# Performance work log

Hardware: AMD Instinct MI355X
Metric: run time of the kernel (lower is better)

## Reference

```python
import jax, jax.numpy as jnp
import numpy as np

T = 3              # num_ntype (slots)
NH = 64            # num_hidden == num_classes
HEADS = (4, 4, 1)
NUM_ETYPES = 5
EDGE_DIM = 64
N_NODES = 20000
NEG_SLOPE = 0.2
ALPHA = 0.05       # residual-attention blend
EPS = 1e-12


def _l2_by_slot(x):
    # l2_norm with l2BySlot='True': normalize each ntype slot independently
    n = x.shape[0]
    xs = x.reshape(n, T, -1)
    nrm = jnp.linalg.norm(xs, axis=2, keepdims=True)
    return (xs / jnp.maximum(nrm, EPS)).reshape(n, -1)


def _edge_softmax(logits, dst, n):
    # softmax over incoming edges of each destination node
    m = jax.lax.stop_gradient(jax.ops.segment_max(logits, dst, num_segments=n))
    e = jnp.exp(logits - m[dst])
    s = jax.ops.segment_sum(e, dst, num_segments=n)
    return e / s[dst]


def _conv(x, src, dst, etype, W, al, ar, ee_tab, We, ae, res_attn, act):
    # slotGATConv: x [N,T,C], W [T,C,H*O], al/ar [H,T*O], ee_tab [R,De], We [De,H*De], ae [H,De]
    n = x.shape[0]
    H = al.shape[0]
    proj = jnp.einsum('ntc,tcd->ntd', x, W)                     # [N,T,H*O]
    O = proj.shape[-1] // H
    feat = proj.reshape(n, T, H, O).transpose(0, 2, 1, 3).reshape(n, H, T * O)
    el = jnp.einsum('nhd,hd->nh', feat, al)
    er = jnp.einsum('nhd,hd->nh', feat, ar)
    De = ee_tab.shape[1]
    ep = (ee_tab[etype] @ We).reshape(-1, H, De)                # [E,H,De]
    ee = jnp.einsum('ehd,hd->eh', ep, ae)                       # [E,H]
    logit = jax.nn.leaky_relu(el[src] + er[dst] + ee, NEG_SLOPE)
    a = _edge_softmax(logit, dst, n)                            # [E,H]
    if res_attn is not None:
        a = a * (1.0 - ALPHA) + res_attn * ALPHA
    out = jax.ops.segment_sum(feat[src] * a[:, :, None], dst, num_segments=n)  # [N,H,T*O]
    if act:
        out = jax.nn.elu(out)
    return out, a


def _forward(feat0, feat1, feat2, w_in0, b_in0, w_in1, b_in1, w_in2, b_in2,
             l0_W, l0_al, l0_ar, l0_ee, l0_we, l0_ae,
             l1_W, l1_al, l1_ar, l1_ee, l1_we, l1_ae,
             l2_W, l2_al, l2_ar, l2_ee, l2_we, l2_ae,
             dm_W, e_feat, src, dst, left, right, mid):
    feats = [feat0, feat1, feat2]
    lins = [(w_in0, b_in0), (w_in1, b_in1), (w_in2, b_in2)]
    blocks = []
    for t, (f, (w, b)) in enumerate(zip(feats, lins)):
        ft = f @ w + b                                          # [n_t, NH]
        pad = jnp.zeros((f.shape[0], T * NH), ft.dtype)
        blocks.append(pad.at[:, t * NH:(t + 1) * NH].set(ft))   # slot zero-padding
    h = jnp.concatenate(blocks, 0)                              # [N, T*NH]
    emb = [_l2_by_slot(h)]                                      # aggregator='None' -> identity
    x = h.reshape(-1, T, NH)
    out0, a0 = _conv(x, src, dst, e_feat, l0_W, l0_al, l0_ar, l0_ee, l0_we, l0_ae, None, True)
    emb.append(_l2_by_slot(out0.mean(1)))
    x = out0.reshape(-1, HEADS[0], T, NH).transpose(0, 2, 1, 3).reshape(-1, T, HEADS[0] * NH)
    out1, a1 = _conv(x, src, dst, e_feat, l1_W, l1_al, l1_ar, l1_ee, l1_we, l1_ae, a0, True)
    emb.append(_l2_by_slot(out1.mean(1)))
    x = out1.reshape(-1, HEADS[1], T, NH).transpose(0, 2, 1, 3).reshape(-1, T, HEADS[1] * NH)
    out2, _ = _conv(x, src, dst, e_feat, l2_W, l2_al, l2_ar, l2_ee, l2_we, l2_ae, a1, False)
    emb.append(_l2_by_slot(out2.mean(1)))
    # aggregator='None' + inProcessEmb='True': concat per-slot along feature dim
    embs = [e.reshape(-1, T, NH) for e in emb]
    o = jnp.concatenate(embs, 2).reshape(-1, T * NH * len(embs))  # [N, 768]
    le, re = o[left], o[right]
    scores = jnp.zeros(left.shape[0], o.dtype)
    for r in range(NUM_ETYPES):                                 # DistMult per relation
        s = ((le @ dm_W[r]) * re).sum(1)
        scores = jnp.where(mid == r, s, scores)
    return jax.nn.sigmoid(scores)


def setup_inputs() -> dict:
    key = jax.random.key(0)
    ks = iter(jax.random.split(key, 64))
    def nrm(shape, std):
        return jax.random.normal(next(ks), shape, jnp.float32) * std
    counts = [8000, 6000, 6000]
    in_dims = [256, 128, 64]
    inp = {}
    for t in range(T):
        inp[f'feat{t}'] = jax.random.normal(next(ks), (counts[t], in_dims[t]), jnp.float32)
        inp[f'w_in{t}'] = nrm((in_dims[t], NH), 0.1)
        inp[f'b_in{t}'] = nrm((NH,), 0.1)
    Cs = [NH, HEADS[0] * NH, HEADS[1] * NH]
    for l in range(3):
        H = HEADS[l]
        inp[f'l{l}_W'] = nrm((T, Cs[l], H * NH), 0.1)
        inp[f'l{l}_al'] = nrm((H, T * NH), 0.1)
        inp[f'l{l}_ar'] = nrm((H, T * NH), 0.1)
        inp[f'l{l}_ee'] = nrm((NUM_ETYPES, EDGE_DIM), 0.1)
        inp[f'l{l}_we'] = nrm((EDGE_DIM, H * EDGE_DIM), 0.1)
        inp[f'l{l}_ae'] = nrm((H, EDGE_DIM), 0.1)
    D = T * NH * 4
    inp['dm_W'] = nrm((NUM_ETYPES, D, D), 0.05)
    E, L = 200000, 10000
    inp['e_feat'] = jax.random.randint(next(ks), (E,), 0, NUM_ETYPES)
    inp['src'] = jax.random.randint(next(ks), (E,), 0, N_NODES)
    inp['dst'] = jax.random.randint(next(ks), (E,), 0, N_NODES)
    inp['left'] = jax.random.randint(next(ks), (L,), 0, N_NODES)
    inp['right'] = jax.random.randint(next(ks), (L,), 0, N_NODES)
    inp['mid'] = jax.random.randint(next(ks), (L,), 0, NUM_ETYPES)
    return inp


def reference(feat0, feat1, feat2, w_in0, b_in0, w_in1, b_in1, w_in2, b_in2,
              l0_W, l0_al, l0_ar, l0_ee, l0_we, l0_ae,
              l1_W, l1_al, l1_ar, l1_ee, l1_we, l1_ae,
              l2_W, l2_al, l2_ar, l2_ee, l2_we, l2_ae,
              dm_W, e_feat, src, dst, left, right, mid):
    return _forward(feat0, feat1, feat2, w_in0, b_in0, w_in1, b_in1, w_in2, b_in2,
                    l0_W, l0_al, l0_ar, l0_ee, l0_we, l0_ae,
                    l1_W, l1_al, l1_ar, l1_ee, l1_we, l1_ae,
                    l2_W, l2_al, l2_ar, l2_ee, l2_we, l2_ae,
                    dm_W, e_feat, src, dst, left, right, mid)
```

## Files before the change

kernel.cpp:

```cpp
#include <hip/hip_runtime.h>
#include <math.h>

#define N_NODES 20000
#define NPAD    20096
#define N_EDGES 200000
#define N_PAIRS 10000
#define PAIR_PAD 10368
#define DM_TILES 162
#define NBLK    79

typedef __attribute__((ext_vector_type(8))) short s16x8;
typedef __attribute__((ext_vector_type(4))) float f32x4;

__device__ inline float wave_max(float v){
  for (int o = 32; o > 0; o >>= 1) v = fmaxf(v, __shfl_xor(v, o));
  return v;
}
__device__ inline float wave_sum(float v){
  for (int o = 32; o > 0; o >>= 1) v += __shfl_xor(v, o);
  return v;
}
__device__ inline short f2bf(float x){
  union { float f; unsigned u; } v; v.f = x;
  unsigned r = (v.u + 0x7FFFu + ((v.u >> 16) & 1u)) >> 16;
  return (short)r;
}
__device__ inline float bf2f(short s){
  union { unsigned u; float f; } v; v.u = ((unsigned)(unsigned short)s) << 16;
  return v.f;
}

__global__ void build_h(const float* __restrict__ f0, const float* __restrict__ w0, const float* __restrict__ b0,
                        const float* __restrict__ f1, const float* __restrict__ w1, const float* __restrict__ b1,
                        const float* __restrict__ f2, const float* __restrict__ w2, const float* __restrict__ b2,
                        short* __restrict__ Xb0, short* __restrict__ o_b){
  int n = blockIdx.x, lane = threadIdx.x;
  int t, idx, C; const float *f, *w, *b;
  if (n < 8000)       { t = 0; idx = n;         C = 256; f = f0; w = w0; b = b0; }
  else if (n < 14000) { t = 1; idx = n - 8000;  C = 128; f = f1; w = w1; b = b1; }
  else                { t = 2; idx = n - 14000; C = 64;  f = f2; w = w2; b = b2; }
  __shared__ float xs[256];
  for (int c = lane; c < C; c += 64) xs[c] = f[(size_t)idx * C + c];
  __syncthreads();
  float acc = b[lane];
  for (int c = 0; c < C; c++) acc += xs[c] * w[c * 64 + lane];
  for (int tt = 0; tt < 3; tt++)
    Xb0[((size_t)(tt * NPAD) + n) * 64 + lane] = f2bf((tt == t) ? acc : 0.f);
  float ss = wave_sum(acc * acc);
  float sc = 1.f / fmaxf(sqrtf(ss), 1e-12f);
  for (int tt = 0; tt < 3; tt++)
    o_b[(size_t)n * 768 + tt * 256 + lane] = f2bf((tt == t) ? acc * sc : 0.f);
}

__global__ void zero_init(int* __restrict__ csr_cnt, int* __restrict__ cnt5, int* __restrict__ pos5,
                          float* __restrict__ score, int* __restrict__ pairs,
                          short* __restrict__ Xb0, short* __restrict__ Xb12){
  int i = blockIdx.x * 256 + threadIdx.x;
  if (i < N_NODES) csr_cnt[i] = 0;
  if (i < 5) { cnt5[i * 16] = 0; pos5[i * 16] = 0; }
  if (i < N_PAIRS) score[i] = 0.f;
  if (i < PAIR_PAD) pairs[i] = -1;
  s16x8 z = {};
  if (i < 4608){
    int t = (i * 16) / 24576, off = (i * 16) % 24576;
    short* p = Xb12 + ((size_t)(t * NPAD + N_NODES)) * 256 + off;
    *(s16x8*)p = z; *(s16x8*)(p + 8) = z;
  }
  if (i < 1152){
    int t = (i * 16) / 6144, off = (i * 16) % 6144;
    short* p = Xb0 + ((size_t)(t * NPAD + N_NODES)) * 64 + off;
    *(s16x8*)p = z; *(s16x8*)(p + 8) = z;
  }
}

__global__ void count_k(const int* __restrict__ dst, int* __restrict__ csr_cnt,
                        const int* __restrict__ mid, int* __restrict__ cnt5){
  int e = blockIdx.x * 256 + threadIdx.x;
  int lane = threadIdx.x & 63;
  if (e < N_EDGES) atomicAdd(&csr_cnt[dst[e]], 1);
  int r_mine = (e < N_PAIRS) ? mid[e] : -1;
#pragma unroll
  for (int r = 0; r < 5; r++){
    unsigned long long mask = __ballot(r_mine == r);
    if (mask){
      int leader = __ffsll((long long)mask) - 1;
      if (lane == leader) atomicAdd(&cnt5[r * 16], __popcll(mask));
    }
  }
}

__global__ void scan1_k(const int* __restrict__ cnt, int* __restrict__ loc, int* __restrict__ bsum){
  __shared__ int s[256];
  int tid = threadIdx.x;
  int idx = blockIdx.x * 256 + tid;
  int v = (idx < N_NODES) ? cnt[idx] : 0;
  s[tid] = v;
  __syncthreads();
  for (int o = 1; o < 256; o <<= 1){
    int u = (tid >= o) ? s[tid - o] : 0;
    __syncthreads();
    s[tid] += u;
    __syncthreads();
  }
  if (idx < N_NODES) loc[idx] = s[tid] - v;
  if (tid == 255) bsum[blockIdx.x] = s[255];
}

__global__ void scan2_k(const int* __restrict__ bsum, int* __restrict__ bofs,
                        const int* __restrict__ cnt5, int* __restrict__ off5){
  __shared__ int s[128];
  int tid = threadIdx.x;
  int v = (tid < NBLK) ? bsum[tid] : 0;
  s[tid] = v;
  __syncthreads();
  for (int o = 1; o < 128; o <<= 1){
    int u = (tid >= o) ? s[tid - o] : 0;
    __syncthreads();
    s[tid] += u;
    __syncthreads();
  }
  if (tid < NBLK) bofs[tid] = s[tid] - v;
  if (tid == 0){
    int r0 = 0;
    for (int r = 0; r < 5; r++){ off5[r] = r0; r0 += ((cnt5[r * 16] + 63) >> 6) << 6; }
  }
}

__global__ void scan3_k(const int* __restrict__ loc, const int* __restrict__ bofs,
                        int* __restrict__ coff, int* __restrict__ cpos){
  int idx = blockIdx.x * 256 + threadIdx.x;
  if (idx < N_NODES){
    int v = loc[idx] + bofs[blockIdx.x];
    coff[idx] = v;
    cpos[idx * 16] = v;
  }
  if (idx == 0) coff[N_NODES] = N_EDGES;
}

__global__ void scatter_k(const int* __restrict__ dst, const int* __restrict__ srcv,
                          const int* __restrict__ efeat, int* __restrict__ cpos,
                          int* __restrict__ src_sorted, int* __restrict__ et_sorted,
                          const int* __restrict__ mid, const int* __restrict__ off5,
                          int* __restrict__ pos5, int* __restrict__ pairs){
  int e = blockIdx.x * 256 + threadIdx.x;
  int lane = threadIdx.x & 63;
  if (e < N_EDGES){
    int p = atomicAdd(&cpos[dst[e] * 16], 1);
    src_sorted[p] = srcv[e];
    et_sorted[p] = efeat[e];
  }
  int r_mine = (e < N_PAIRS) ? mid[e] : -1;
#pragma unroll
  for (int r = 0; r < 5; r++){
    unsigned long long mask = __ballot(r_mine == r);
    if (mask){
      int cnt = __popcll(mask);
      int leader = __ffsll((long long)mask) - 1;
      int base = 0;
      if (lane == leader) base = atomicAdd(&pos5[r * 16], cnt);
      base = __shfl(base, leader);
      if (r_mine == r){
        int rank = __popcll(mask & ((1ull << lane) - 1ull));
        pairs[off5[r] + base + rank] = e;
      }
    }
  }
}

__global__ void ee5_all(const float* __restrict__ ee0, const float* __restrict__ we0, const float* __restrict__ ae0,
                        const float* __restrict__ ee1, const float* __restrict__ we1, const float* __restrict__ ae1,
                        const float* __restrict__ ee2, const float* __restrict__ we2, const float* __restrict__ ae2,
                        float* __restrict__ ee5f){
  int r = blockIdx.x, L = blockIdx.y;
  int H = (L == 2) ? 1 : 4;
  const float* eetab = (L == 0) ? ee0 : ((L == 1) ? ee1 : ee2);
  const float* We    = (L == 0) ? we0 : ((L == 1) ? we1 : we2);
  const float* ae    = (L == 0) ? ae0 : ((L == 1) ? ae1 : ae2);
  int h = threadIdx.x >> 6, lane = threadIdx.x & 63;
  if (h >= H) return;
  float v = 0.f;
  for (int k = 0; k < 64; k++) v += eetab[r * 64 + k] * We[k * H * 64 + h * 64 + lane];
  v *= ae[h * 64 + lane];
  v = wave_sum(v);
  if (lane == 0) ee5f[L * 32 + r * H + h] = v;
}

__global__ void transpose_bf16(const float* __restrict__ src, short* __restrict__ dst, int R, int Cc){
  __shared__ float tile[32][33];
  const float* s = src + (size_t)blockIdx.z * R * Cc;
  short* d = dst + (size_t)blockIdx.z * R * Cc;
  int r0 = blockIdx.x * 32, c0 = blockIdx.y * 32;
  int tx = threadIdx.x & 31, ty = threadIdx.x >> 5;
  for (int i = 0; i < 32; i += 8){
    int r = r0 + ty + i;
    tile[ty + i][tx] = (r < R && c0 + tx < Cc) ? s[(size_t)r * Cc + c0 + tx] : 0.f;
  }
  __syncthreads();
  for (int i = 0; i < 32; i += 8){
    int c = c0 + ty + i;
    if (c < Cc && r0 + tx < R)
      d[(size_t)c * R + r0 + tx] = f2bf(tile[tx][ty + i]);
  }
}

template<int C, int NO>
__global__ void mfma_proj(const short* __restrict__ Xb, const short* __restrict__ Wt,
                          short* __restrict__ featb){
  constexpr int H = NO / 64;
  const int n0 = blockIdx.x * 128;
  const int ct = blockIdx.y;
  const int t  = blockIdx.z;
  const int tid = threadIdx.x;
  const int w = tid >> 6, lane = tid & 63;
  const int quad = lane >> 4, ln = lane & 15;
  __shared__ __attribute__((aligned(16))) short A_s[128 * 32];
  __shared__ __attribute__((aligned(16))) short B_s[64 * 32];
  const short* Xt  = Xb + (size_t)t * NPAD * C;
  const short* Wtt = Wt + ((size_t)t * NO + ct * 64) * C;
  f32x4 acc[2][4] = {};
  for (int kk = 0; kk < C; kk += 32){
    {
      int row = tid >> 1, half = tid & 1;
      const s16x8* g = (const s16x8*)(Xt + (size_t)(n0 + row) * C + kk + half * 16);
      s16x8 v0 = g[0], v1 = g[1];
      *(s16x8*)(A_s + row * 32 + half * 16) = v0;
      *(s16x8*)(A_s + row * 32 + half * 16 + 8) = v1;
    }
    {
      int row = tid >> 2, chunk = tid & 3;
      s16x8 v = *(const s16x8*)(Wtt + (size_t)row * C + kk + chunk * 8);
      *(s16x8*)(B_s + row * 32 + chunk * 8) = v;
    }
    __syncthreads();
    s16x8 af0 = *(s16x8*)(A_s + (w * 32 + ln) * 32 + quad * 8);
    s16x8 af1 = *(s16x8*)(A_s + (w * 32 + 16 + ln) * 32 + quad * 8);
    s16x8 bf[4];
#pragma unroll
    for (int b = 0; b < 4; b++) bf[b] = *(s16x8*)(B_s + (b * 16 + ln) * 32 + quad * 8);
#pragma unroll
    for (int b = 0; b < 4; b++){
      acc[0][b] = __builtin_amdgcn_mfma_f32_16x16x32_bf16(af0, bf[b], acc[0][b], 0, 0, 0);
      acc[1][b] = __builtin_amdgcn_mfma_f32_16x16x32_bf16(af1, bf[b], acc[1][b], 0, 0, 0);
    }
    __syncthreads();
  }
#pragma unroll
  for (int ar = 0; ar < 2; ar++){
#pragma unroll
    for (int i = 0; i < 4; i++){
      int n = n0 + w * 32 + ar * 16 + quad * 4 + i;
      if (n >= N_NODES) continue;
#pragma unroll
      for (int b = 0; b < 4; b++){
        int d = ct * 64 + b * 16 + ln;
        int h = d >> 6, jj = d & 63;
        featb[((size_t)n * H + h) * 192 + t * 64 + jj] = f2bf(acc[ar][b][i]);
      }
    }
  }
}

__global__ void elr_kernel(const short* __restrict__ featb, const float* __restrict__ al,
                           const float* __restrict__ ar, float* __restrict__ el,
                           float* __restrict__ er, int H, int total){
  int wid = threadIdx.x >> 6, lane = threadIdx.x & 63;
  int gw = blockIdx.x * 4 + wid;
  if (gw >= total) return;
  int h = gw % H;
  const short* f = featb + (size_t)gw * 192;
  float sl = 0.f, sr = 0.f;
  for (int i = 0; i < 3; i++){
    int dd = i * 64 + lane;
    float v = bf2f(f[dd]);
    sl += v * al[h * 192 + dd];
    sr += v * ar[h * 192 + dd];
  }
  sl = wave_sum(sl); sr = wave_sum(sr);
  if (lane == 0){ el[gw] = sl; er[gw] = sr; }
}

template<int H, int MODE>
__global__ __launch_bounds__(256) void softmax_k(
    const int* __restrict__ csr_off, const int* __restrict__ src_sorted,
    const int* __restrict__ et_sorted,
    const float* __restrict__ el, const float* __restrict__ er, const float* __restrict__ ee5,
    const float* __restrict__ aprev, float* __restrict__ aout){
  const int wid = threadIdx.x >> 6, lane = threadIdx.x & 63;
  const int n = blockIdx.x * 4 + wid;
  if (n >= N_NODES) return;
  const int off = csr_off[n];
  const int cnt = csr_off[n + 1] - off;
  if (cnt == 0) return;
  float ern[H];
#pragma unroll
  for (int h = 0; h < H; h++) ern[h] = er[n * H + h];
  if (cnt <= 64){
    int p = off + lane;
    int sidx = 0, r = 0;
    if (lane < cnt){ sidx = src_sorted[p]; r = et_sorted[p]; }
    float lg[H];
#pragma unroll
    for (int h = 0; h < H; h++) lg[h] = -1e30f;
    if (lane < cnt){
#pragma unroll
      for (int h = 0; h < H; h++){
        float v = el[sidx * H + h] + ern[h] + ee5[r * H + h];
        lg[h] = (v >= 0.f) ? v : 0.2f * v;
      }
    }
    float ap[4] = {};
    if (MODE > 0 && lane < cnt){
#pragma unroll
      for (int q = 0; q < 4; q++) ap[q] = aprev[(size_t)p * 4 + q];
    }
    float av[H];
#pragma unroll
    for (int h = 0; h < H; h++){
      float mh = wave_max(lg[h]);
      float ex = (lane < cnt) ? __expf(lg[h] - mh) : 0.f;
      float sh = wave_sum(ex);
      float a = ex / sh;
      if (MODE == 1) a = 0.95f * a + 0.05f * ap[h];
      if (MODE == 2) a = 0.95f * a + 0.0125f * (ap[0] + ap[1] + ap[2] + ap[3]);
      av[h] = a;
    }
    if (lane < cnt){
      if (H == 4){
        f32x4 o = {av[0], av[1], av[2], av[3]};
        *(f32x4*)(aout + (size_t)p * 4) = o;
      } else {
        aout[p] = av[0];
      }
    }
  } else {
    float mh[H], sh[H];
#pragma unroll
    for (int h = 0; h < H; h++){ mh[h] = -1e30f; sh[h] = 0.f; }
    for (int b = lane; b < cnt; b += 64){
      int p = off + b; int s = src_sorted[p]; int r = et_sorted[p];
#pragma unroll
      for (int h = 0; h < H; h++){
        float v = el[s * H + h] + ern[h] + ee5[r * H + h];
        v = (v >= 0.f) ? v : 0.2f * v;
        mh[h] = fmaxf(mh[h], v);
      }
    }
#pragma unroll
    for (int h = 0; h < H; h++) mh[h] = wave_max(mh[h]);
    for (int b = lane; b < cnt; b += 64){
      int p = off + b; int s = src_sorted[p]; int r = et_sorted[p];
#pragma unroll
      for (int h = 0; h < H; h++){
        float v = el[s * H + h] + ern[h] + ee5[r * H + h];
        v = (v >= 0.f) ? v : 0.2f * v;
        sh[h] += __expf(v - mh[h]);
      }
    }
#pragma unroll
    for (int h = 0; h < H; h++) sh[h] = wave_sum(sh[h]);
    for (int b = lane; b < cnt; b += 64){
      int p = off + b; int s = src_sorted[p]; int r = et_sorted[p];
      float ap[4] = {};
      if (MODE > 0){
#pragma unroll
        for (int q = 0; q < 4; q++) ap[q] = aprev[(size_t)p * 4 + q];
      }
      float av[H];
#pragma unroll
      for (int h = 0; h < H; h++){
        float v = el[s * H + h] + ern[h] + ee5[r * H + h];
        v = (v >= 0.f) ? v : 0.2f * v;
        float a = __expf(v - mh[h]) / sh[h];
        if (MODE == 1) a = 0.95f * a + 0.05f * ap[h];
        if (MODE == 2) a = 0.95f * a + 0.0125f * (ap[0] + ap[1] + ap[2] + ap[3]);
        av[h] = a;
      }
      if (H == 4){
        f32x4 o = {av[0], av[1], av[2], av[3]};
        *(f32x4*)(aout + (size_t)p * 4) = o;
      } else {
        aout[p] = av[0];
      }
    }
  }
}

template<int H, int ACT>
__global__ __launch_bounds__(256) void agg_row(
    const int* __restrict__ csr_off, const int* __restrict__ src_sorted,
    const float* __restrict__ aW, const short* __restrict__ featb,
    short* __restrict__ outb, short* __restrict__ o_b, int kslice){
  const int wid = threadIdx.x >> 6, lane = threadIdx.x & 63;
  const int n = blockIdx.x * 4 + wid;
  if (n >= N_NODES) return;
  constexpr int NC = H * 192 / 8;
  const int c0 = lane, h0 = (c0 / 24) % H;
  const int c1 = lane + 64, h1 = (c1 / 24) % H;
  const bool act0 = (c0 < NC);
  const bool act1 = (H == 4) && (lane < 32);
  const int off = csr_off[n];
  const int cnt = csr_off[n + 1] - off;
  __shared__ float out_s[4][H * 192];
  float acc0[8] = {}, acc1[8] = {};
  int b = 0;
  for (; b + 4 <= cnt; b += 4){
    int p = off + b;
    int s0 = src_sorted[p],     s1 = src_sorted[p + 1];
    int s2 = src_sorted[p + 2], s3 = src_sorted[p + 3];
    float a00, a01, a02, a03, a10, a11, a12, a13;
    if (H == 4){
      a00 = aW[(size_t)p * 4 + h0];       a01 = aW[(size_t)(p + 1) * 4 + h0];
      a02 = aW[(size_t)(p + 2) * 4 + h0]; a03 = aW[(size_t)(p + 3) * 4 + h0];
      a10 = aW[(size_t)p * 4 + h1];       a11 = aW[(size_t)(p + 1) * 4 + h1];
      a12 = aW[(size_t)(p + 2) * 4 + h1]; a13 = aW[(size_t)(p + 3) * 4 + h1];
    } else {
      a00 = aW[p]; a01 = aW[p + 1]; a02 = aW[p + 2]; a03 = aW[p + 3];
      a10 = a11 = a12 = a13 = 0.f;
    }
    s16x8 v00, v01, v02, v03, v10, v11, v12, v13;
    if (act0){
      v00 = *(const s16x8*)(featb + (size_t)s0 * (H * 192) + c0 * 8);
      v01 = *(const s16x8*)(featb + (size_t)s1 * (H * 192) + c0 * 8);
      v02 = *(const s16x8*)(featb + (size_t)s2 * (H * 192) + c0 * 8);
      v03 = *(const s16x8*)(featb + (size_t)s3 * (H * 192) + c0 * 8);
    }
    if (act1){
      v10 = *(const s16x8*)(featb + (size_t)s0 * (H * 192) + c1 * 8);
      v11 = *(const s16x8*)(featb + (size_t)s1 * (H * 192) + c1 * 8);
      v12 = *(const s16x8*)(featb + (size_t)s2 * (H * 192) + c1 * 8);
      v13 = *(const s16x8*)(featb + (size_t)s3 * (H * 192) + c1 * 8);
    }
    if (act0){
#pragma unroll
      for (int i = 0; i < 8; i++)
        acc0[i] += a00 * bf2f(v00[i]) + a01 * bf2f(v01[i]) +
                   a02 * bf2f(v02[i]) + a03 * bf2f(v03[i]);
    }
    if (act1){
#pragma unroll
      for (int i = 0; i < 8; i++)
        acc1[i] += a10 * bf2f(v10[i]) + a11 * bf2f(v11[i]) +
                   a12 * bf2f(v12[i]) + a13 * bf2f(v13[i]);
    }
  }
  for (; b < cnt; b++){
    int p = off + b;
    int s = src_sorted[p];
    if (act0){
      float a = (H == 4) ? aW[(size_t)p * 4 + h0] : aW[p];
      s16x8 v = *(const s16x8*)(featb + (size_t)s * (H * 192) + c0 * 8);
#pragma unroll
      for (int i = 0; i < 8; i++) acc0[i] += a * bf2f(v[i]);
    }
    if (act1){
      float a = aW[(size_t)p * 4 + h1];
      s16x8 v = *(const s16x8*)(featb + (size_t)s * (H * 192) + c1 * 8);
#pragma unroll
      for (int i = 0; i < 8; i++) acc1[i] += a * bf2f(v[i]);
    }
  }
  if (act0){
    int dd = c0 * 8, h = dd / 192, rr = dd % 192, t = rr / 64, j = rr % 64;
    if (ACT){
#pragma unroll
      for (int i = 0; i < 8; i++) acc0[i] = (acc0[i] > 0.f) ? acc0[i] : expm1f(acc0[i]);
    }
#pragma unroll
    for (int i = 0; i < 8; i++) out_s[wid][dd + i] = acc0[i];
    if (outb){
      s16x8 o;
#pragma unroll
      for (int i = 0; i < 8; i++) o[i] = f2bf(acc0[i]);
      *(s16x8*)(outb + ((size_t)(t * NPAD) + n) * 256 + h * 64 + j) = o;
    }
  }
  if (act1){
    int dd = c1 * 8, h = dd / 192, rr = dd % 192, t = rr / 64, j = rr % 64;
    if (ACT){
#pragma unroll
      for (int i = 0; i < 8; i++) acc1[i] = (acc1[i] > 0.f) ? acc1[i] : expm1f(acc1[i]);
    }
#pragma unroll
    for (int i = 0; i < 8; i++) out_s[wid][dd + i] = acc1[i];
    if (outb){
      s16x8 o;
#pragma unroll
      for (int i = 0; i < 8; i++) o[i] = f2bf(acc1[i]);
      *(s16x8*)(outb + ((size_t)(t * NPAD) + n) * 256 + h * 64 + j) = o;
    }
  }
  for (int t = 0; t < 3; t++){
    float v;
    if (H == 4)
      v = 0.25f * (out_s[wid][t * 64 + lane] + out_s[wid][192 + t * 64 + lane] +
                   out_s[wid][384 + t * 64 + lane] + out_s[wid][576 + t * 64 + lane]);
    else
      v = out_s[wid][t * 64 + lane];
    float ss = wave_sum(v * v);
    float sc = 1.f / fmaxf(sqrtf(ss), 1e-12f);
    o_b[(size_t)n * 768 + t * 256 + kslice * 64 + lane] = f2bf(v * sc);
  }
}

__global__ void distmult_mfma(const short* __restrict__ o_b, const short* __restrict__ Mt,
                              const int* __restrict__ pairs, const int* __restrict__ left,
                              const int* __restrict__ right, const int* __restrict__ mid,
                              float* __restrict__ score){
  const int pt = blockIdx.x, ct = blockIdx.y;
  const int tid = threadIdx.x;
  const int w = tid >> 6, lane = tid & 63;
  const int quad = lane >> 4, ln = lane & 15;
// ... 53 lines not shown
  }
  __syncthreads();
#pragma unroll
  for (int i = 0; i < 4; i++){
    int row = w * 16 + quad * 4 + i;
    float s = 0.f;
#pragma unroll
    for (int b = 0; b < 8; b++)
      s += acc[b][i] * bf2f(RE_s[row * 128 + b * 16 + ln]);
    s += __shfl_xor(s, 1); s += __shfl_xor(s, 2);
    s += __shfl_xor(s, 4); s += __shfl_xor(s, 8);
    if (ln == 0){
      int p = pid_s[row];
      if (p >= 0) atomicAdd(&score[p], s);
    }
  }
}

__global__ void sigmoid_k(const float* __restrict__ score, float* __restrict__ out){
  int i = blockIdx.x * 256 + threadIdx.x;
  if (i < N_PAIRS) out[i] = 1.f / (1.f + __expf(-score[i]));
}

extern "C" void kernel_launch(void* const* d_in, const int* in_sizes, int n_in,
                              void* d_out, int out_size, void* d_ws, size_t ws_size,
                              hipStream_t stream){
  const float* f0 = (const float*)d_in[0];
  const float* w0 = (const float*)d_in[1];
  const float* b0 = (const float*)d_in[2];
  const float* f1 = (const float*)d_in[3];
  const float* w1 = (const float*)d_in[4];
  const float* b1 = (const float*)d_in[5];
  const float* f2 = (const float*)d_in[6];
  const float* w2_ = (const float*)d_in[7];
  const float* b2 = (const float*)d_in[8];
  const float* lW[3]  = {(const float*)d_in[9],  (const float*)d_in[15], (const float*)d_in[21]};
  const float* lal[3] = {(const float*)d_in[10], (const float*)d_in[16], (const float*)d_in[22]};
  const float* lar[3] = {(const float*)d_in[11], (const float*)d_in[17], (const float*)d_in[23]};
  const float* lee[3] = {(const float*)d_in[12], (const float*)d_in[18], (const float*)d_in[24]};
  const float* lwe[3] = {(const float*)d_in[13], (const float*)d_in[19], (const float*)d_in[25]};
  const float* lae[3] = {(const float*)d_in[14], (const float*)d_in[20], (const float*)d_in[26]};
  const float* dmW = (const float*)d_in[27];
  const int* efeat = (const int*)d_in[28];
  const int* srcv  = (const int*)d_in[29];
  const int* dstv  = (const int*)d_in[30];
  const int* left  = (const int*)d_in[31];
  const int* right = (const int*)d_in[32];
  const int* midv  = (const int*)d_in[33];
  float* out = (float*)d_out;

  short* feat_b = (short*)d_ws;
  float* aA     = (float*)(feat_b + 15360000);
  float* aB     = aA + 800000;
  float* w2b    = aB + 800000;
  float* elf    = w2b + 200000;
  float* erf    = elf + 80000;
  float* ee5f   = erf + 80000;
  float* score  = ee5f + 96;
  int* csr_cnt  = (int*)(score + 10016);
  int* csr_off  = csr_cnt + 20000;
  int* csr_pos  = csr_off + 20004;
  int* loc      = csr_pos + 320000;
  int* bsum     = loc + 20000;
  int* bofs     = bsum + 128;
  int* src_sorted = bofs + 128;
  int* et_sorted  = src_sorted + 200000;
  int* cnt5     = et_sorted + 200000;
  int* off5     = cnt5 + 80;
  int* pos5     = off5 + 8;
  int* pairs    = pos5 + 80;
  short* o_b    = (short*)(pairs + PAIR_PAD);
  short* Xb0    = o_b + 15360000;
  short* Xb12   = Xb0 + 3858432;
  short* Wt0    = Xb12 + 15433728;
  short* Wt1    = Wt0 + 49152;
  short* Wt2    = Wt1 + 196608;
  short* Mt     = Wt2 + 49152;

  zero_init<<<80, 256, 0, stream>>>(csr_cnt, cnt5, pos5, score, pairs, Xb0, Xb12);
  build_h<<<N_NODES, 64, 0, stream>>>(f0, w0, b0, f1, w1, b1, f2, w2_, b2, Xb0, o_b);
  count_k<<<782, 256, 0, stream>>>(dstv, csr_cnt, midv, cnt5);
  scan1_k<<<NBLK, 256, 0, stream>>>(csr_cnt, loc, bsum);
  scan2_k<<<1, 128, 0, stream>>>(bsum, bofs, cnt5, off5);
  scan3_k<<<NBLK, 256, 0, stream>>>(loc, bofs, csr_off, csr_pos);
  scatter_k<<<782, 256, 0, stream>>>(dstv, srcv, efeat, csr_pos, src_sorted, et_sorted,
                                     midv, off5, pos5, pairs);
  { dim3 g(5, 3); ee5_all<<<g, 256, 0, stream>>>(lee[0], lwe[0], lae[0], lee[1], lwe[1], lae[1],
                                                 lee[2], lwe[2], lae[2], ee5f); }

  { dim3 g(2, 8, 3);   transpose_bf16<<<g, 256, 0, stream>>>(lW[0], Wt0, 64, 256); }
  { dim3 g(8, 8, 3);   transpose_bf16<<<g, 256, 0, stream>>>(lW[1], Wt1, 256, 256); }
  { dim3 g(8, 2, 3);   transpose_bf16<<<g, 256, 0, stream>>>(lW[2], Wt2, 256, 64); }
  { dim3 g(24, 24, 5); transpose_bf16<<<g, 256, 0, stream>>>(dmW, Mt, 768, 768); }

  { dim3 g(NPAD / 128, 4, 3); mfma_proj<64, 256><<<g, 256, 0, stream>>>(Xb0, Wt0, feat_b); }
  elr_kernel<<<20000, 256, 0, stream>>>(feat_b, lal[0], lar[0], elf, erf, 4, 80000);
  softmax_k<4, 0><<<5000, 256, 0, stream>>>(csr_off, src_sorted, et_sorted, elf, erf, ee5f,
                                            nullptr, aA);
  agg_row<4, 1><<<5000, 256, 0, stream>>>(csr_off, src_sorted, aA, feat_b, Xb12, o_b, 1);

  { dim3 g(NPAD / 128, 4, 3); mfma_proj<256, 256><<<g, 256, 0, stream>>>(Xb12, Wt1, feat_b); }
  elr_kernel<<<20000, 256, 0, stream>>>(feat_b, lal[1], lar[1], elf, erf, 4, 80000);
  softmax_k<4, 1><<<5000, 256, 0, stream>>>(csr_off, src_sorted, et_sorted, elf, erf, ee5f + 32,
                                            aA, aB);
  agg_row<4, 1><<<5000, 256, 0, stream>>>(csr_off, src_sorted, aB, feat_b, Xb12, o_b, 2);

  { dim3 g(NPAD / 128, 1, 3); mfma_proj<256, 64><<<g, 256, 0, stream>>>(Xb12, Wt2, feat_b); }
  elr_kernel<<<5000, 256, 0, stream>>>(feat_b, lal[2], lar[2], elf, erf, 1, 20000);
  softmax_k<1, 2><<<5000, 256, 0, stream>>>(csr_off, src_sorted, et_sorted, elf, erf, ee5f + 64,
                                            aB, w2b);
  agg_row<1, 0><<<5000, 256, 0, stream>>>(csr_off, src_sorted, w2b, feat_b, nullptr, o_b, 3);

  { dim3 g(DM_TILES, 6); distmult_mfma<<<g, 256, 0, stream>>>(o_b, Mt, pairs, left, right, midv, score); }
  sigmoid_k<<<40, 256, 0, stream>>>(score, out);
}
```

Measured before the change: 536.9 us.

## Fuse GAT softmax with aggregation, attention logits into projection, merge prep kernels

```diff
diff --git a/kernel.cpp b/kernel.cpp
--- a/kernel.cpp
+++ b/kernel.cpp
@@ -33,8 +33,28 @@
 __global__ void build_h(const float* __restrict__ f0, const float* __restrict__ w0, const float* __restrict__ b0,
                         const float* __restrict__ f1, const float* __restrict__ w1, const float* __restrict__ b1,
                         const float* __restrict__ f2, const float* __restrict__ w2, const float* __restrict__ b2,
-                        short* __restrict__ Xb0, short* __restrict__ o_b){
+                        short* __restrict__ Xb0, short* __restrict__ o_b,
+                        int* __restrict__ csr_cnt, int* __restrict__ cnt5, int* __restrict__ pos5,
+                        float* __restrict__ score, int* __restrict__ pairs,
+                        float* __restrict__ eall, short* __restrict__ Xb12){
   int n = blockIdx.x, lane = threadIdx.x;
+  int idx64 = n * 64 + lane;
+  if (lane == 0) csr_cnt[n] = 0;
+  if (n == 0 && lane < 5){ cnt5[lane * 16] = 0; pos5[lane * 16] = 0; }
+  if (idx64 < N_PAIRS + 16 && idx64 < 10016) score[idx64] = 0.f;
+  if (idx64 < PAIR_PAD) pairs[idx64] = -1;
+  if (idx64 < 480000) eall[idx64] = 0.f;
+  s16x8 z = {};
+  if (idx64 < 4608){
+    int t = (idx64 * 16) / 24576, off = (idx64 * 16) % 24576;
+    short* p = Xb12 + ((size_t)(t * NPAD + N_NODES)) * 256 + off;
+    *(s16x8*)p = z; *(s16x8*)(p + 8) = z;
+  }
+  if (idx64 < 1152){
+    int t = (idx64 * 16) / 6144, off = (idx64 * 16) % 6144;
+    short* p = Xb0 + ((size_t)(t * NPAD + N_NODES)) * 64 + off;
+    *(s16x8*)p = z; *(s16x8*)(p + 8) = z;
+  }
   int t, idx, C; const float *f, *w, *b;
   if (n < 8000)       { t = 0; idx = n;         C = 256; f = f0; w = w0; b = b0; }
   else if (n < 14000) { t = 1; idx = n - 8000;  C = 128; f = f1; w = w1; b = b1; }
@@ -52,27 +72,6 @@
     o_b[(size_t)n * 768 + tt * 256 + lane] = f2bf((tt == t) ? acc * sc : 0.f);
 }
 
-__global__ void zero_init(int* __restrict__ csr_cnt, int* __restrict__ cnt5, int* __restrict__ pos5,
-                          float* __restrict__ score, int* __restrict__ pairs,
-                          short* __restrict__ Xb0, short* __restrict__ Xb12){
-  int i = blockIdx.x * 256 + threadIdx.x;
-  if (i < N_NODES) csr_cnt[i] = 0;
-  if (i < 5) { cnt5[i * 16] = 0; pos5[i * 16] = 0; }
-  if (i < N_PAIRS) score[i] = 0.f;
-  if (i < PAIR_PAD) pairs[i] = -1;
-  s16x8 z = {};
-  if (i < 4608){
-    int t = (i * 16) / 24576, off = (i * 16) % 24576;
-    short* p = Xb12 + ((size_t)(t * NPAD + N_NODES)) * 256 + off;
-    *(s16x8*)p = z; *(s16x8*)(p + 8) = z;
-  }
-  if (i < 1152){
-    int t = (i * 16) / 6144, off = (i * 16) % 6144;
-    short* p = Xb0 + ((size_t)(t * NPAD + N_NODES)) * 64 + off;
-    *(s16x8*)p = z; *(s16x8*)(p + 8) = z;
-  }
-}
-
 __global__ void count_k(const int* __restrict__ dst, int* __restrict__ csr_cnt,
                         const int* __restrict__ mid, int* __restrict__ cnt5){
   int e = blockIdx.x * 256 + threadIdx.x;
@@ -167,29 +166,52 @@
   }
 }
 
-__global__ void ee5_all(const float* __restrict__ ee0, const float* __restrict__ we0, const float* __restrict__ ae0,
-                        const float* __restrict__ ee1, const float* __restrict__ we1, const float* __restrict__ ae1,
-                        const float* __restrict__ ee2, const float* __restrict__ we2, const float* __restrict__ ae2,
-                        float* __restrict__ ee5f){
-  int r = blockIdx.x, L = blockIdx.y;
-  int H = (L == 2) ? 1 : 4;
-  const float* eetab = (L == 0) ? ee0 : ((L == 1) ? ee1 : ee2);
-  const float* We    = (L == 0) ? we0 : ((L == 1) ? we1 : we2);
-  const float* ae    = (L == 0) ? ae0 : ((L == 1) ? ae1 : ae2);
-  int h = threadIdx.x >> 6, lane = threadIdx.x & 63;
-  if (h >= H) return;
-  float v = 0.f;
-  for (int k = 0; k < 64; k++) v += eetab[r * 64 + k] * We[k * H * 64 + h * 64 + lane];
-  v *= ae[h * 64 + lane];
-  v = wave_sum(v);
-  if (lane == 0) ee5f[L * 32 + r * H + h] = v;
-}
-
-__global__ void transpose_bf16(const float* __restrict__ src, short* __restrict__ dst, int R, int Cc){
+__global__ void prep_k(const float* __restrict__ lW0, const float* __restrict__ lW1,
+                       const float* __restrict__ lW2, const float* __restrict__ dmW,
+                       short* __restrict__ Wt0, short* __restrict__ Wt1,
+                       short* __restrict__ Wt2, short* __restrict__ Mt,
+                       const float* __restrict__ ee0, const float* __restrict__ we0, const float* __restrict__ ae0,
+                       const float* __restrict__ ee1, const float* __restrict__ we1, const float* __restrict__ ae1,
+                       const float* __restrict__ ee2, const float* __restrict__ we2, const float* __restrict__ ae2,
+                       float* __restrict__ ee5f){
+  const int bx = blockIdx.x, by = blockIdx.y, z = blockIdx.z;
+  if (z == 10){
+    int r = bx, L = by;
+    if (r >= 5 || L >= 3) return;
+    int H = (L == 2) ? 1 : 4;
+    const float* eetab = (L == 0) ? ee0 : ((L == 1) ? ee1 : ee2);
+    const float* We    = (L == 0) ? we0 : ((L == 1) ? we1 : we2);
+    const float* ae    = (L == 0) ? ae0 : ((L == 1) ? ae1 : ae2);
+    int h = threadIdx.x >> 6, lane = threadIdx.x & 63;
+    if (h >= H) return;
+    float v = 0.f;
+    for (int k = 0; k < 64; k++) v += eetab[r * 64 + k] * We[k * H * 64 + h * 64 + lane];
+    v *= ae[h * 64 + lane];
+    v = wave_sum(v);
+    if (lane == 0) ee5f[L * 32 + r * H + h] = v;
+    return;
+  }
+  const float* s; short* d; int R, Cc, r0, c0;
+  if (z < 5){
+    s = dmW + (size_t)z * 589824; d = Mt + (size_t)z * 589824;
+    R = 768; Cc = 768; r0 = bx * 32; c0 = by * 32;
+  } else if (z < 8){
+    if (bx >= 8 || by >= 8) return;
+    int t = z - 5;
+    s = lW1 + (size_t)t * 65536; d = Wt1 + (size_t)t * 65536;
+    R = 256; Cc = 256; r0 = bx * 32; c0 = by * 32;
+  } else if (z == 8){
+    if (bx >= 6 || by >= 8) return;
+    int t = bx >> 1;
+    s = lW0 + (size_t)t * 16384; d = Wt0 + (size_t)t * 16384;
+    R = 64; Cc = 256; r0 = (bx & 1) * 32; c0 = by * 32;
+  } else {
+    if (bx >= 8 || by >= 6) return;
+    int t = by >> 1;
+    s = lW2 + (size_t)t * 16384; d = Wt2 + (size_t)t * 16384;
+    R = 256; Cc = 64; r0 = bx * 32; c0 = (by & 1) * 32;
+  }
   __shared__ float tile[32][33];
-  const float* s = src + (size_t)blockIdx.z * R * Cc;
-  short* d = dst + (size_t)blockIdx.z * R * Cc;
-  int r0 = blockIdx.x * 32, c0 = blockIdx.y * 32;
   int tx = threadIdx.x & 31, ty = threadIdx.x >> 5;
   for (int i = 0; i < 32; i += 8){
     int r = r0 + ty + i;
@@ -205,7 +227,9 @@
 
 template<int C, int NO>
 __global__ void mfma_proj(const short* __restrict__ Xb, const short* __restrict__ Wt,
-                          short* __restrict__ featb){
+                          short* __restrict__ featb, const float* __restrict__ al,
+                          const float* __restrict__ ar, float* __restrict__ elf,
+                          float* __restrict__ erf){
   constexpr int H = NO / 64;
   const int n0 = blockIdx.x * 128;
   const int ct = blockIdx.y;
@@ -245,151 +269,56 @@
     __syncthreads();
   }
 #pragma unroll
-  for (int ar = 0; ar < 2; ar++){
+  for (int ar_ = 0; ar_ < 2; ar_++){
 #pragma unroll
     for (int i = 0; i < 4; i++){
-      int n = n0 + w * 32 + ar * 16 + quad * 4 + i;
+      int n = n0 + w * 32 + ar_ * 16 + quad * 4 + i;
       if (n >= N_NODES) continue;
 #pragma unroll
       for (int b = 0; b < 4; b++){
-        int d = ct * 64 + b * 16 + ln;
-        int h = d >> 6, jj = d & 63;
-        featb[((size_t)n * H + h) * 192 + t * 64 + jj] = f2bf(acc[ar][b][i]);
-      }
-    }
-  }
-}
-
-__global__ void elr_kernel(const short* __restrict__ featb, const float* __restrict__ al,
-                           const float* __restrict__ ar, float* __restrict__ el,
-                           float* __restrict__ er, int H, int total){
-  int wid = threadIdx.x >> 6, lane = threadIdx.x & 63;
-  int gw = blockIdx.x * 4 + wid;
-  if (gw >= total) return;
-  int h = gw % H;
-  const short* f = featb + (size_t)gw * 192;
-  float sl = 0.f, sr = 0.f;
-  for (int i = 0; i < 3; i++){
-    int dd = i * 64 + lane;
-    float v = bf2f(f[dd]);
-    sl += v * al[h * 192 + dd];
-    sr += v * ar[h * 192 + dd];
-  }
-  sl = wave_sum(sl); sr = wave_sum(sr);
-  if (lane == 0){ el[gw] = sl; er[gw] = sr; }
-}
-
-template<int H, int MODE>
-__global__ __launch_bounds__(256) void softmax_k(
+        int jj = b * 16 + ln;
+        featb[((size_t)n * H + ct) * 192 + t * 64 + jj] = f2bf(acc[ar_][b][i]);
+      }
+    }
+  }
+  float alv[4], arv[4];
+#pragma unroll
+  for (int b = 0; b < 4; b++){
+    alv[b] = al[ct * 192 + t * 64 + b * 16 + ln];
+    arv[b] = ar[ct * 192 + t * 64 + b * 16 + ln];
+  }
+#pragma unroll
+  for (int ar_ = 0; ar_ < 2; ar_++){
+#pragma unroll
+    for (int i = 0; i < 4; i++){
+      float pe = 0.f, pr = 0.f;
+#pragma unroll
+      for (int b = 0; b < 4; b++){
+        pe += acc[ar_][b][i] * alv[b];
+        pr += acc[ar_][b][i] * arv[b];
+      }
+#pragma unroll
+      for (int o = 1; o < 16; o <<= 1){
+        pe += __shfl_xor(pe, o);
+        pr += __shfl_xor(pr, o);
+      }
+      int n = n0 + w * 32 + ar_ * 16 + quad * 4 + i;
+      if (ln == 0 && n < N_NODES){
+        atomicAdd(&elf[n * H + ct], pe);
+        atomicAdd(&erf[n * H + ct], pr);
+      }
+    }
+  }
+}
+
+template<int H, int MODE, int ACT>
+__global__ __launch_bounds__(256) void gat_fused(
     const int* __restrict__ csr_off, const int* __restrict__ src_sorted,
     const int* __restrict__ et_sorted,
     const float* __restrict__ el, const float* __restrict__ er, const float* __restrict__ ee5,
-    const float* __restrict__ aprev, float* __restrict__ aout){
-  const int wid = threadIdx.x >> 6, lane = threadIdx.x & 63;
-  const int n = blockIdx.x * 4 + wid;
-  if (n >= N_NODES) return;
-  const int off = csr_off[n];
-  const int cnt = csr_off[n + 1] - off;
-  if (cnt == 0) return;
-  float ern[H];
-#pragma unroll
-  for (int h = 0; h < H; h++) ern[h] = er[n * H + h];
-  if (cnt <= 64){
-    int p = off + lane;
-    int sidx = 0, r = 0;
-    if (lane < cnt){ sidx = src_sorted[p]; r = et_sorted[p]; }
-    float lg[H];
-#pragma unroll
-    for (int h = 0; h < H; h++) lg[h] = -1e30f;
-    if (lane < cnt){
-#pragma unroll
-      for (int h = 0; h < H; h++){
-        float v = el[sidx * H + h] + ern[h] + ee5[r * H + h];
-        lg[h] = (v >= 0.f) ? v : 0.2f * v;
-      }
-    }
-    float ap[4] = {};
-    if (MODE > 0 && lane < cnt){
-#pragma unroll
-      for (int q = 0; q < 4; q++) ap[q] = aprev[(size_t)p * 4 + q];
-    }
-    float av[H];
-#pragma unroll
-    for (int h = 0; h < H; h++){
-      float mh = wave_max(lg[h]);
-      float ex = (lane < cnt) ? __expf(lg[h] - mh) : 0.f;
-      float sh = wave_sum(ex);
-      float a = ex / sh;
-      if (MODE == 1) a = 0.95f * a + 0.05f * ap[h];
-      if (MODE == 2) a = 0.95f * a + 0.0125f * (ap[0] + ap[1] + ap[2] + ap[3]);
-      av[h] = a;
-    }
-    if (lane < cnt){
-      if (H == 4){
-        f32x4 o = {av[0], av[1], av[2], av[3]};
-        *(f32x4*)(aout + (size_t)p * 4) = o;
-      } else {
-        aout[p] = av[0];
-      }
-    }
-  } else {
-    float mh[H], sh[H];
-#pragma unroll
-    for (int h = 0; h < H; h++){ mh[h] = -1e30f; sh[h] = 0.f; }
-    for (int b = lane; b < cnt; b += 64){
-      int p = off + b; int s = src_sorted[p]; int r = et_sorted[p];
-#pragma unroll
-      for (int h = 0; h < H; h++){
-        float v = el[s * H + h] + ern[h] + ee5[r * H + h];
-        v = (v >= 0.f) ? v : 0.2f * v;
-        mh[h] = fmaxf(mh[h], v);
-      }
-    }
-#pragma unroll
-    for (int h = 0; h < H; h++) mh[h] = wave_max(mh[h]);
-    for (int b = lane; b < cnt; b += 64){
-      int p = off + b; int s = src_sorted[p]; int r = et_sorted[p];
-#pragma unroll
-      for (int h = 0; h < H; h++){
-        float v = el[s * H + h] + ern[h] + ee5[r * H + h];
-        v = (v >= 0.f) ? v : 0.2f * v;
-        sh[h] += __expf(v - mh[h]);
-      }
-    }
-#pragma unroll
-    for (int h = 0; h < H; h++) sh[h] = wave_sum(sh[h]);
-    for (int b = lane; b < cnt; b += 64){
-      int p = off + b; int s = src_sorted[p]; int r = et_sorted[p];
-      float ap[4] = {};
-      if (MODE > 0){
-#pragma unroll
-        for (int q = 0; q < 4; q++) ap[q] = aprev[(size_t)p * 4 + q];
-      }
-      float av[H];
-#pragma unroll
-      for (int h = 0; h < H; h++){
-        float v = el[s * H + h] + ern[h] + ee5[r * H + h];
-        v = (v >= 0.f) ? v : 0.2f * v;
-        float a = __expf(v - mh[h]) / sh[h];
-        if (MODE == 1) a = 0.95f * a + 0.05f * ap[h];
-        if (MODE == 2) a = 0.95f * a + 0.0125f * (ap[0] + ap[1] + ap[2] + ap[3]);
-        av[h] = a;
-      }
-      if (H == 4){
-        f32x4 o = {av[0], av[1], av[2], av[3]};
-        *(f32x4*)(aout + (size_t)p * 4) = o;
-      } else {
-        aout[p] = av[0];
-      }
-    }
-  }
-}
-
-template<int H, int ACT>
-__global__ __launch_bounds__(256) void agg_row(
-    const int* __restrict__ csr_off, const int* __restrict__ src_sorted,
-    const float* __restrict__ aW, const short* __restrict__ featb,
-    short* __restrict__ outb, short* __restrict__ o_b, int kslice){
+    const float* __restrict__ aprev, float* __restrict__ aout,
+    const short* __restrict__ featb, short* __restrict__ outb,
+    short* __restrict__ o_b, int kslice){
   const int wid = threadIdx.x >> 6, lane = threadIdx.x & 63;
   const int n = blockIdx.x * 4 + wid;
   if (n >= N_NODES) return;
@@ -400,63 +329,173 @@
   const bool act1 = (H == 4) && (lane < 32);
   const int off = csr_off[n];
   const int cnt = csr_off[n + 1] - off;
+  __shared__ float a_s[4][64][H];
   __shared__ float out_s[4][H * 192];
   float acc0[8] = {}, acc1[8] = {};
-  int b = 0;
-  for (; b + 4 <= cnt; b += 4){
-    int p = off + b;
-    int s0 = src_sorted[p],     s1 = src_sorted[p + 1];
-    int s2 = src_sorted[p + 2], s3 = src_sorted[p + 3];
-    float a00, a01, a02, a03, a10, a11, a12, a13;
-    if (H == 4){
-      a00 = aW[(size_t)p * 4 + h0];       a01 = aW[(size_t)(p + 1) * 4 + h0];
-      a02 = aW[(size_t)(p + 2) * 4 + h0]; a03 = aW[(size_t)(p + 3) * 4 + h0];
-      a10 = aW[(size_t)p * 4 + h1];       a11 = aW[(size_t)(p + 1) * 4 + h1];
-      a12 = aW[(size_t)(p + 2) * 4 + h1]; a13 = aW[(size_t)(p + 3) * 4 + h1];
-    } else {
-      a00 = aW[p]; a01 = aW[p + 1]; a02 = aW[p + 2]; a03 = aW[p + 3];
-      a10 = a11 = a12 = a13 = 0.f;
-    }
-    s16x8 v00, v01, v02, v03, v10, v11, v12, v13;
-    if (act0){
-      v00 = *(const s16x8*)(featb + (size_t)s0 * (H * 192) + c0 * 8);
-      v01 = *(const s16x8*)(featb + (size_t)s1 * (H * 192) + c0 * 8);
-      v02 = *(const s16x8*)(featb + (size_t)s2 * (H * 192) + c0 * 8);
-      v03 = *(const s16x8*)(featb + (size_t)s3 * (H * 192) + c0 * 8);
-    }
-    if (act1){
-      v10 = *(const s16x8*)(featb + (size_t)s0 * (H * 192) + c1 * 8);
-      v11 = *(const s16x8*)(featb + (size_t)s1 * (H * 192) + c1 * 8);
-      v12 = *(const s16x8*)(featb + (size_t)s2 * (H * 192) + c1 * 8);
-      v13 = *(const s16x8*)(featb + (size_t)s3 * (H * 192) + c1 * 8);
-    }
-    if (act0){
-#pragma unroll
-      for (int i = 0; i < 8; i++)
-        acc0[i] += a00 * bf2f(v00[i]) + a01 * bf2f(v01[i]) +
-                   a02 * bf2f(v02[i]) + a03 * bf2f(v03[i]);
-    }
-    if (act1){
-#pragma unroll
-      for (int i = 0; i < 8; i++)
-        acc1[i] += a10 * bf2f(v10[i]) + a11 * bf2f(v11[i]) +
-                   a12 * bf2f(v12[i]) + a13 * bf2f(v13[i]);
-    }
-  }
-  for (; b < cnt; b++){
-    int p = off + b;
-    int s = src_sorted[p];
-    if (act0){
-      float a = (H == 4) ? aW[(size_t)p * 4 + h0] : aW[p];
-      s16x8 v = *(const s16x8*)(featb + (size_t)s * (H * 192) + c0 * 8);
-#pragma unroll
-      for (int i = 0; i < 8; i++) acc0[i] += a * bf2f(v[i]);
-    }
-    if (act1){
-      float a = aW[(size_t)p * 4 + h1];
-      s16x8 v = *(const s16x8*)(featb + (size_t)s * (H * 192) + c1 * 8);
-#pragma unroll
-      for (int i = 0; i < 8; i++) acc1[i] += a * bf2f(v[i]);
+  float ern[H];
+#pragma unroll
+  for (int h = 0; h < H; h++) ern[h] = er[n * H + h];
+
+  if (cnt > 0 && cnt <= 64){
+    int p = off + lane;
+    int sidx = 0, r = 0;
+    if (lane < cnt){ sidx = src_sorted[p]; r = et_sorted[p]; }
+    float lg[H];
+#pragma unroll
+    for (int h = 0; h < H; h++) lg[h] = -1e30f;
+    if (lane < cnt){
+#pragma unroll
+      for (int h = 0; h < H; h++){
+        float v = el[sidx * H + h] + ern[h] + ee5[r * H + h];
+        lg[h] = (v >= 0.f) ? v : 0.2f * v;
+      }
+    }
+    float ap[4] = {};
+    if (MODE > 0 && lane < cnt){
+#pragma unroll
+      for (int q = 0; q < 4; q++) ap[q] = aprev[(size_t)p * 4 + q];
+    }
+    float av[H];
+#pragma unroll
+    for (int h = 0; h < H; h++){
+      float mh = wave_max(lg[h]);
+      float ex = (lane < cnt) ? __expf(lg[h] - mh) : 0.f;
+      float sh = wave_sum(ex);
+      float a = ex / sh;
+      if (MODE == 1) a = 0.95f * a + 0.05f * ap[h];
+      if (MODE == 2) a = 0.95f * a + 0.0125f * (ap[0] + ap[1] + ap[2] + ap[3]);
+      av[h] = a;
+      if (lane < cnt) a_s[wid][lane][h] = a;
+    }
+    if (MODE != 2 && lane < cnt){
+      f32x4 o = {av[0], av[1], av[2], av[3]};
+      *(f32x4*)(aout + (size_t)p * 4) = o;
+    }
+    int b = 0;
+    for (; b + 4 <= cnt; b += 4){
+      int p4 = off + b;
+      int s0 = src_sorted[p4],     s1 = src_sorted[p4 + 1];
+      int s2 = src_sorted[p4 + 2], s3 = src_sorted[p4 + 3];
+      s16x8 v00, v01, v02, v03, v10, v11, v12, v13;
+      if (act0){
+        v00 = *(const s16x8*)(featb + (size_t)s0 * (H * 192) + c0 * 8);
+        v01 = *(const s16x8*)(featb + (size_t)s1 * (H * 192) + c0 * 8);
+        v02 = *(const s16x8*)(featb + (size_t)s2 * (H * 192) + c0 * 8);
+        v03 = *(const s16x8*)(featb + (size_t)s3 * (H * 192) + c0 * 8);
+      }
+      if (act1){
+        v10 = *(const s16x8*)(featb + (size_t)s0 * (H * 192) + c1 * 8);
+        v11 = *(const s16x8*)(featb + (size_t)s1 * (H * 192) + c1 * 8);
+        v12 = *(const s16x8*)(featb + (size_t)s2 * (H * 192) + c1 * 8);
+        v13 = *(const s16x8*)(featb + (size_t)s3 * (H * 192) + c1 * 8);
+      }
+      if (act0){
+        float a0 = a_s[wid][b][h0], a1 = a_s[wid][b + 1][h0];
+        float a2 = a_s[wid][b + 2][h0], a3 = a_s[wid][b + 3][h0];
+#pragma unroll
+        for (int i = 0; i < 8; i++)
+          acc0[i] += a0 * bf2f(v00[i]) + a1 * bf2f(v01[i]) +
+                     a2 * bf2f(v02[i]) + a3 * bf2f(v03[i]);
+      }
+      if (act1){
+        float a0 = a_s[wid][b][h1], a1 = a_s[wid][b + 1][h1];
+        float a2 = a_s[wid][b + 2][h1], a3 = a_s[wid][b + 3][h1];
+#pragma unroll
+        for (int i = 0; i < 8; i++)
+          acc1[i] += a0 * bf2f(v10[i]) + a1 * bf2f(v11[i]) +
+                     a2 * bf2f(v12[i]) + a3 * bf2f(v13[i]);
+      }
+    }
+    for (; b < cnt; b++){
+      int pp = off + b;
+      int s = src_sorted[pp];
+      if (act0){
+        float a = a_s[wid][b][h0];
+        s16x8 v = *(const s16x8*)(featb + (size_t)s * (H * 192) + c0 * 8);
+#pragma unroll
+        for (int i = 0; i < 8; i++) acc0[i] += a * bf2f(v[i]);
+      }
+      if (act1){
+        float a = a_s[wid][b][h1];
+        s16x8 v = *(const s16x8*)(featb + (size_t)s * (H * 192) + c1 * 8);
+#pragma unroll
+        for (int i = 0; i < 8; i++) acc1[i] += a * bf2f(v[i]);
+      }
+    }
+  } else if (cnt > 64){
+    float mh[H], sh[H];
+#pragma unroll
+    for (int h = 0; h < H; h++){ mh[h] = -1e30f; sh[h] = 0.f; }
+    for (int b = lane; b < cnt; b += 64){
+      int p = off + b; int s = src_sorted[p]; int r = et_sorted[p];
+#pragma unroll
+      for (int h = 0; h < H; h++){
+        float v = el[s * H + h] + ern[h] + ee5[r * H + h];
+        v = (v >= 0.f) ? v : 0.2f * v;
+        mh[h] = fmaxf(mh[h], v);
+      }
+    }
+#pragma unroll
+    for (int h = 0; h < H; h++) mh[h] = wave_max(mh[h]);
+    for (int b = lane; b < cnt; b += 64){
+      int p = off + b; int s = src_sorted[p]; int r = et_sorted[p];
+#pragma unroll
+      for (int h = 0; h < H; h++){
+        float v = el[s * H + h] + ern[h] + ee5[r * H + h];
+        v = (v >= 0.f) ? v : 0.2f * v;
+        sh[h] += __expf(v - mh[h]);
+      }
+    }
+#pragma unroll
+    for (int h = 0; h < H; h++) sh[h] = wave_sum(sh[h]);
+    if (MODE != 2){
+      for (int b = lane; b < cnt; b += 64){
+        int p = off + b; int s = src_sorted[p]; int r = et_sorted[p];
+        float ap[4] = {};
+        if (MODE > 0){
+#pragma unroll
+          for (int q = 0; q < 4; q++) ap[q] = aprev[(size_t)p * 4 + q];
+        }
+        float av[4] = {};
+#pragma unroll
+        for (int h = 0; h < H; h++){
+          float v = el[s * H + h] + ern[h] + ee5[r * H + h];
+          v = (v >= 0.f) ? v : 0.2f * v;
+          float a = __expf(v - mh[h]) / sh[h];
+          if (MODE == 1) a = 0.95f * a + 0.05f * ap[h];
+          av[h] = a;
+        }
+        f32x4 o = {av[0], av[1], av[2], av[3]};
+        *(f32x4*)(aout + (size_t)p * 4) = o;
+      }
+    }
+    for (int b = 0; b < cnt; b++){
+      int p = off + b; int s = src_sorted[p]; int r = et_sorted[p];
+      const short* row = featb + (size_t)s * (H * 192);
+      float apm[4] = {};
+      if (MODE > 0){
+#pragma unroll
+        for (int q = 0; q < 4; q++) apm[q] = aprev[(size_t)p * 4 + q];
+      }
+      if (act0){
+        float v = el[s * H + h0] + ern[h0] + ee5[r * H + h0];
+        v = (v >= 0.f) ? v : 0.2f * v;
+        float a = __expf(v - mh[h0]) / sh[h0];
+        if (MODE == 1) a = 0.95f * a + 0.05f * apm[h0];
+        if (MODE == 2) a = 0.95f * a + 0.0125f * (apm[0] + apm[1] + apm[2] + apm[3]);
+        s16x8 vv = *(const s16x8*)(row + c0 * 8);
+#pragma unroll
+        for (int i = 0; i < 8; i++) acc0[i] += a * bf2f(vv[i]);
+      }
+      if (act1){
+        float v = el[s * H + h1] + ern[h1] + ee5[r * H + h1];
+        v = (v >= 0.f) ? v : 0.2f * v;
+        float a = __expf(v - mh[h1]) / sh[h1];
+        if (MODE == 1) a = 0.95f * a + 0.05f * apm[h1];
+        s16x8 vv = *(const s16x8*)(row + c1 * 8);
+#pragma unroll
+        for (int i = 0; i < 8; i++) acc1[i] += a * bf2f(vv[i]);
+      }
     }
   }
   if (act0){
@@ -616,10 +655,8 @@
   short* feat_b = (short*)d_ws;
   float* aA     = (float*)(feat_b + 15360000);
   float* aB     = aA + 800000;
-  float* w2b    = aB + 800000;
-  float* elf    = w2b + 200000;
-  float* erf    = elf + 80000;
-  float* ee5f   = erf + 80000;
+  float* eall   = aB + 800000;
+  float* ee5f   = eall + 480000;
   float* score  = ee5f + 96;
   int* csr_cnt  = (int*)(score + 10016);
   int* csr_off  = csr_cnt + 20000;
@@ -640,40 +677,37 @@
   short* Wt1    = Wt0 + 49152;
   short* Wt2    = Wt1 + 196608;
   short* Mt     = Wt2 + 49152;
-
-  zero_init<<<80, 256, 0, stream>>>(csr_cnt, cnt5, pos5, score, pairs, Xb0, Xb12);
-  build_h<<<N_NODES, 64, 0, stream>>>(f0, w0, b0, f1, w1, b1, f2, w2_, b2, Xb0, o_b);
+  float* elf0 = eall, *erf0 = eall + 80000;
+  float* elf1 = eall + 160000, *erf1 = eall + 240000;
+  float* elf2 = eall + 320000, *erf2 = eall + 400000;
+
+  build_h<<<N_NODES, 64, 0, stream>>>(f0, w0, b0, f1, w1, b1, f2, w2_, b2, Xb0, o_b,
+                                      csr_cnt, cnt5, pos5, score, pairs, eall, Xb12);
   count_k<<<782, 256, 0, stream>>>(dstv, csr_cnt, midv, cnt5);
   scan1_k<<<NBLK, 256, 0, stream>>>(csr_cnt, loc, bsum);
   scan2_k<<<1, 128, 0, stream>>>(bsum, bofs, cnt5, off5);
   scan3_k<<<NBLK, 256, 0, stream>>>(loc, bofs, csr_off, csr_pos);
   scatter_k<<<782, 256, 0, stream>>>(dstv, srcv, efeat, csr_pos, src_sorted, et_sorted,
                                      midv, off5, pos5, pairs);
-  { dim3 g(5, 3); ee5_all<<<g, 256, 0, stream>>>(lee[0], lwe[0], lae[0], lee[1], lwe[1], lae[1],
-                                                 lee[2], lwe[2], lae[2], ee5f); }
-
-  { dim3 g(2, 8, 3);   transpose_bf16<<<g, 256, 0, stream>>>(lW[0], Wt0, 64, 256); }
-  { dim3 g(8, 8, 3);   transpose_bf16<<<g, 256, 0, stream>>>(lW[1], Wt1, 256, 256); }
-  { dim3 g(8, 2, 3);   transpose_bf16<<<g, 256, 0, stream>>>(lW[2], Wt2, 256, 64); }
-  { dim3 g(24, 24, 5); transpose_bf16<<<g, 256, 0, stream>>>(dmW, Mt, 768, 768); }
-
-  { dim3 g(NPAD / 128, 4, 3); mfma_proj<64, 256><<<g, 256, 0, stream>>>(Xb0, Wt0, feat_b); }
-  elr_kernel<<<20000, 256, 0, stream>>>(feat_b, lal[0], lar[0], elf, erf, 4, 80000);
-  softmax_k<4, 0><<<5000, 256, 0, stream>>>(csr_off, src_sorted, et_sorted, elf, erf, ee5f,
-                                            nullptr, aA);
-  agg_row<4, 1><<<5000, 256, 0, stream>>>(csr_off, src_sorted, aA, feat_b, Xb12, o_b, 1);
-
-  { dim3 g(NPAD / 128, 4, 3); mfma_proj<256, 256><<<g, 256, 0, stream>>>(Xb12, Wt1, feat_b); }
-  elr_kernel<<<20000, 256, 0, stream>>>(feat_b, lal[1], lar[1], elf, erf, 4, 80000);
-  softmax_k<4, 1><<<5000, 256, 0, stream>>>(csr_off, src_sorted, et_sorted, elf, erf, ee5f + 32,
-                                            aA, aB);
-  agg_row<4, 1><<<5000, 256, 0, stream>>>(csr_off, src_sorted, aB, feat_b, Xb12, o_b, 2);
-
-  { dim3 g(NPAD / 128, 1, 3); mfma_proj<256, 64><<<g, 256, 0, stream>>>(Xb12, Wt2, feat_b); }
-  elr_kernel<<<5000, 256, 0, stream>>>(feat_b, lal[2], lar[2], elf, erf, 1, 20000);
-  softmax_k<1, 2><<<5000, 256, 0, stream>>>(csr_off, src_sorted, et_sorted, elf, erf, ee5f + 64,
-                                            aB, w2b);
-  agg_row<1, 0><<<5000, 256, 0, stream>>>(csr_off, src_sorted, w2b, feat_b, nullptr, o_b, 3);
+  { dim3 g(24, 24, 11);
+    prep_k<<<g, 256, 0, stream>>>(lW[0], lW[1], lW[2], dmW, Wt0, Wt1, Wt2, Mt,
+                                  lee[0], lwe[0], lae[0], lee[1], lwe[1], lae[1],
+                                  lee[2], lwe[2], lae[2], ee5f); }
+
+  { dim3 g(NPAD / 128, 4, 3);
+    mfma_proj<64, 256><<<g, 256, 0, stream>>>(Xb0, Wt0, feat_b, lal[0], lar[0], elf0, erf0); }
+  gat_fused<4, 0, 1><<<5000, 256, 0, stream>>>(csr_off, src_sorted, et_sorted, elf0, erf0, ee5f,
+                                               nullptr, aA, feat_b, Xb12, o_b, 1);
+
+  { dim3 g(NPAD / 128, 4, 3);
+    mfma_proj<256, 256><<<g, 256, 0, stream>>>(Xb12, Wt1, feat_b, lal[1], lar[1], elf1, erf1); }
+  gat_fused<4, 1, 1><<<5000, 256, 0, stream>>>(csr_off, src_sorted, et_sorted, elf1, erf1, ee5f + 32,
+                                               aA, aB, feat_b, Xb12, o_b, 2);
+
+  { dim3 g(NPAD / 128, 1, 3);
+    mfma_proj<256, 64><<<g, 256, 0, stream>>>(Xb12, Wt2, feat_b, lal[2], lar[2], elf2, erf2); }
+  gat_fused<1, 2, 0><<<5000, 256, 0, stream>>>(csr_off, src_sorted, et_sorted, elf2, erf2, ee5f + 64,
+                                               aB, nullptr, feat_b, nullptr, o_b, 3);
 
   { dim3 g(DM_TILES, 6); distmult_mfma<<<g, 256, 0, stream>>>(o_b, Mt, pairs, left, right, midv, score); }
   sigmoid_k<<<40, 256, 0, stream>>>(score, out);
```

Measured after the change: 530.9 us. Within noise of the previous version (-1.1%).
